# Optimization experiments

Hardware: AMD Instinct MI355X
Metric: run time of the kernel (lower is better)

The kernel has to match this reference:

```python
import jax, jax.numpy as jnp
import numpy as np

HEAD_NUM = 16
ROPE_BASE = 10000.0


def _rotate_half(x):
    # interleaved pairs: (x0,x1,x2,x3,...) -> (-x1,x0,-x3,x2,...)
    x_even = x[..., ::2]
    x_odd = x[..., 1::2]
    return jnp.stack((-x_odd, x_even), axis=-1).reshape(x.shape)


def _rope_cos_sin(seq_len, head_dim):
    half = head_dim // 2
    inv_freq = 1.0 / (ROPE_BASE ** (jnp.arange(half, dtype=jnp.float32) / half))
    t = jnp.arange(seq_len, dtype=jnp.float32)
    freqs = t[:, None] * inv_freq[None, :]            # [S, half]
    cos = jnp.repeat(jnp.cos(freqs), 2, axis=-1)       # [S, D]
    sin = jnp.repeat(jnp.sin(freqs), 2, axis=-1)       # [S, D]
    return cos, sin


def setup_inputs() -> dict:
    key = jax.random.key(0)
    ks = jax.random.split(key, 9)
    B, S, H = 2, 2048, 2048
    std = 1.0 / np.sqrt(H)
    return {
        "x": jax.random.normal(ks[0], (B, S, H), jnp.float32),
        "Wq": jax.random.normal(ks[1], (H, H), jnp.float32) * std,
        "bq": jax.random.normal(ks[2], (H,), jnp.float32) * std,
        "Wk": jax.random.normal(ks[3], (H, H), jnp.float32) * std,
        "bk": jax.random.normal(ks[4], (H,), jnp.float32) * std,
        "Wv": jax.random.normal(ks[5], (H, H), jnp.float32) * std,
        "bv": jax.random.normal(ks[6], (H,), jnp.float32) * std,
        "Wo": jax.random.normal(ks[7], (H, H), jnp.float32) * std,
        "bo": jax.random.normal(ks[8], (H,), jnp.float32) * std,
    }


def reference(x, Wq, bq, Wk, bk, Wv, bv, Wo, bo):
    B, S, H = x.shape
    nh = HEAD_NUM
    d = H // nh
    scale = jnp.float32(np.sqrt(d))

    def proj(W, b):
        y = x @ W.T + b                                 # torch Linear: x W^T + b
        return y.reshape(B, S, nh, d).transpose(0, 2, 1, 3)  # [B, nh, S, d]

    Q = proj(Wq, bq)
    K = proj(Wk, bk)
    V = proj(Wv, bv)

    cos, sin = _rope_cos_sin(S, d)                      # [S, d]
    Q = Q * cos + _rotate_half(Q) * sin
    K = K * cos + _rotate_half(K) * sin

    scores = jnp.einsum("bhqd,bhkd->bhqk", Q, K) / scale  # [B, nh, S, S]
    causal = jnp.tril(jnp.ones((S, S), dtype=bool))
    scores = jnp.where(causal, scores, jnp.float32(-jnp.inf))
    attn = jax.nn.softmax(scores, axis=-1)
    out = jnp.einsum("bhqk,bhkd->bhqd", attn, V)        # [B, nh, S, d]
    out = out.transpose(0, 2, 1, 3).reshape(B, S, H)
    return out @ Wo.T + bo
```

## Files before the change

### kernel.cpp

```cpp
#include <hip/hip_runtime.h>
#include <math.h>

typedef __bf16 bf16x8 __attribute__((ext_vector_type(8)));
typedef float floatx4 __attribute__((ext_vector_type(4)));

__device__ __forceinline__ unsigned short f32_to_bf16(float f) {
  unsigned int u = __float_as_uint(f);
  u = u + 0x7FFFu + ((u >> 16) & 1u);
  return (unsigned short)(u >> 16);
}
__device__ __forceinline__ float bf16_to_f32(unsigned short s) {
  return __uint_as_float(((unsigned int)s) << 16);
}

__device__ __forceinline__ void gld_lds16(const unsigned short* g,
                                          unsigned short* l) {
  __builtin_amdgcn_global_load_lds(
      (const __attribute__((address_space(1))) unsigned int*)g,
      (__attribute__((address_space(3))) unsigned int*)l, 16, 0, 0);
}

__global__ void cast_kernel(const float* __restrict__ in,
                            unsigned short* __restrict__ out, int n4) {
  int i = blockIdx.x * blockDim.x + threadIdx.x;
  if (i >= n4) return;
  const float4 v = reinterpret_cast<const float4*>(in)[i];
  ushort4 o;
  o.x = f32_to_bf16(v.x); o.y = f32_to_bf16(v.y);
  o.z = f32_to_bf16(v.z); o.w = f32_to_bf16(v.w);
  reinterpret_cast<ushort4*>(out)[i] = o;
}

__global__ void rope_table_kernel(float2* __restrict__ tab, int total) {
  int idx = blockIdx.x * blockDim.x + threadIdx.x;
  if (idx >= total) return;
  const int s = idx >> 6, i = idx & 63;
  const float inv = powf(10000.0f, -(float)i * (1.0f / 64.0f));
  const float ang = (float)s * inv;
  tab[idx] = make_float2(cosf(ang), sinf(ang));
}

template <int EPI>
__global__ __launch_bounds__(256) void gemm_fused(
    const unsigned short* __restrict__ A, const unsigned short* __restrict__ B,
    const float* __restrict__ bias, float* __restrict__ Cf,
    unsigned short* __restrict__ Cb, const float2* __restrict__ tab,
    float scl, int M, int N, int K, int S) {
  __shared__ unsigned short As[128 * 64];
  __shared__ unsigned short Bs[128 * 64];
  const int t = threadIdx.x;
  const int lane = t & 63;
  const int w = t >> 6;
  const int bm = blockIdx.y * 128;
  const int bn = blockIdx.x * 128;
  const int wm = (w & 1) * 64;
  const int wn = (w >> 1) * 64;
  const int m16 = lane & 15;
  const int quad = lane >> 4;
  const int key = m16 & 7;

  const int lr = lane >> 3;
  const int lc = ((lane & 7) ^ lr) * 8;

  floatx4 acc[4][4];
#pragma unroll
  for (int i = 0; i < 4; ++i)
#pragma unroll
    for (int j = 0; j < 4; ++j) acc[i][j] = floatx4{0.f, 0.f, 0.f, 0.f};

  const unsigned short* Abase = A + (size_t)(bm + w * 32 + lr) * K + lc;
  const unsigned short* Bbase = B + (size_t)(bn + w * 32 + lr) * K + lc;

  for (int k0 = 0; k0 < K; k0 += 64) {
    __syncthreads();
#pragma unroll
    for (int it = 0; it < 4; ++it) {
      gld_lds16(Abase + (size_t)it * 8 * K + k0, &As[(w * 4 + it) * 512]);
      gld_lds16(Bbase + (size_t)it * 8 * K + k0, &Bs[(w * 4 + it) * 512]);
    }
    __syncthreads();
#pragma unroll
    for (int ks = 0; ks < 64; ks += 32) {
      const int ck = ks >> 3;
      bf16x8 af[4], bfr[4];
#pragma unroll
      for (int i = 0; i < 4; ++i)
        af[i] = *reinterpret_cast<const bf16x8*>(
            &As[(wm + i * 16 + m16) * 64 + ((ck | quad) ^ key) * 8]);
#pragma unroll
      for (int j = 0; j < 4; ++j)
        bfr[j] = *reinterpret_cast<const bf16x8*>(
            &Bs[(wn + j * 16 + m16) * 64 + ((ck | quad) ^ key) * 8]);
#pragma unroll
      for (int i = 0; i < 4; ++i)
#pragma unroll
        for (int j = 0; j < 4; ++j)
          acc[i][j] = __builtin_amdgcn_mfma_f32_16x16x32_bf16(
              af[i], bfr[j], acc[i][j], 0, 0, 0);
    }
  }

#pragma unroll
  for (int i = 0; i < 4; ++i) {
    const int rbase = bm + wm + i * 16 + quad * 4;
#pragma unroll
    for (int j = 0; j < 4; ++j) {
      const int col = bn + wn + j * 16 + m16;
      const float bv = bias[col];
      if (EPI == 0) {
#pragma unroll
        for (int r = 0; r < 4; ++r)
          Cf[(size_t)(rbase + r) * N + col] = acc[i][j][r] + bv;
      } else if (EPI == 1) {
        const int pi = (col & 127) >> 1;
#pragma unroll
        for (int r = 0; r < 4; ++r) {
          const int row = rbase + r;
          const int s = row & (S - 1);
          const float v = acc[i][j][r] + bv;
          const float vp = __shfl_xor(v, 1);
          const float2 cs = tab[s * 64 + pi];
          const float oe = (v * cs.x - vp * cs.y) * scl;
          const float oo = (vp * cs.x + v * cs.y) * scl;
          if ((m16 & 1) == 0) {
            const unsigned pk =
                (unsigned)f32_to_bf16(oe) | ((unsigned)f32_to_bf16(oo) << 16);
            *reinterpret_cast<unsigned*>(Cb + (size_t)row * N + col) = pk;
          }
        }
      } else {
        const int b = rbase >> 11;
        const int s = rbase & (S - 1);
        ushort4 pk;
        pk.x = f32_to_bf16(acc[i][j][0] + bv);
        pk.y = f32_to_bf16(acc[i][j][1] + bv);
        pk.z = f32_to_bf16(acc[i][j][2] + bv);
        pk.w = f32_to_bf16(acc[i][j][3] + bv);
        *reinterpret_cast<ushort4*>(
            Cb + ((size_t)((b << 11) + col)) * S + s) = pk;
      }
    }
  }
}

constexpr int F_BQ = 128, F_BK = 64, F_DH = 128;
constexpr int KS_STR = 136;
constexpr int VS_STR = 72;
constexpr int PS_STR = 72;

__global__ __launch_bounds__(256, 2) void fattn_kernel(
    const unsigned short* __restrict__ Qb, const unsigned short* __restrict__ Kb,
    const unsigned short* __restrict__ Vtb, unsigned short* __restrict__ Ob,
    int S, int H, int nh) {
  __shared__ unsigned short Ks[F_BK * KS_STR];
  __shared__ unsigned short Vts[F_DH * VS_STR];
  __shared__ unsigned short Ps[F_BQ * PS_STR];

  const int t = threadIdx.x;
  const int lane = t & 63;
  const int w = t >> 6;
  const int l15 = lane & 15;
  const int quad = lane >> 4;

  const int i = blockIdx.x;
  const int bh = i & 31;
  const int qt = (i < 256) ? (i >> 5) : (15 - ((i - 256) >> 5));
  const int h = bh & 15;
  const int b = bh >> 4;
  const int q0 = qt * F_BQ;

  const unsigned short* Qrow = Qb + ((size_t)(b * S + q0)) * H + h * F_DH;
  const unsigned short* Krow = Kb + ((size_t)b * S) * H + h * F_DH;
  const unsigned short* Vtrow = Vtb + ((size_t)bh * F_DH) * S;
  unsigned short* Orow = Ob + ((size_t)(b * S + q0)) * H + h * F_DH;

  bf16x8 aq[2][4];
#pragma unroll
  for (int qg = 0; qg < 2; ++qg)
#pragma unroll
    for (int ks = 0; ks < 4; ++ks)
      aq[qg][ks] = *reinterpret_cast<const bf16x8*>(
          Qrow + (size_t)(w * 32 + qg * 16 + l15) * H + ks * 32 + quad * 8);

  floatx4 oacc[2][8];
#pragma unroll
  for (int qg = 0; qg < 2; ++qg)
#pragma unroll
    for (int dj = 0; dj < 8; ++dj) oacc[qg][dj] = floatx4{0.f, 0.f, 0.f, 0.f};
  float lpart[2][4] = {{0.f, 0.f, 0.f, 0.f}, {0.f, 0.f, 0.f, 0.f}};
  int qrow[2][4];
#pragma unroll
  for (int qg = 0; qg < 2; ++qg)
#pragma unroll
    for (int r = 0; r < 4; ++r)
      qrow[qg][r] = q0 + w * 32 + qg * 16 + quad * 4 + r;

  const int ntile = q0 / F_BK + 2;
  for (int tile = 0; tile < ntile; ++tile) {
    const int k0 = tile * F_BK;
    __syncthreads();
    {
      const int kt = t >> 2, c0 = (t & 3) * 32;
      const unsigned short* g = Krow + (size_t)(k0 + kt) * H + c0;
#pragma unroll
      for (int ii = 0; ii < 4; ++ii)
        *reinterpret_cast<uint4*>(&Ks[kt * KS_STR + c0 + ii * 8]) =
            *reinterpret_cast<const uint4*>(g + ii * 8);
    }
    {
      const int d = t >> 1, c0 = (t & 1) * 32;
      const unsigned short* g = Vtrow + (size_t)d * S + k0 + c0;
#pragma unroll
      for (int ii = 0; ii < 4; ++ii)
        *reinterpret_cast<uint4*>(&Vts[d * VS_STR + c0 + ii * 8]) =
            *reinterpret_cast<const uint4*>(g + ii * 8);
    }
    __syncthreads();

    floatx4 sacc[2][4];
#pragma unroll
    for (int qg = 0; qg < 2; ++qg)
#pragma unroll
      for (int j = 0; j < 4; ++j) sacc[qg][j] = floatx4{0.f, 0.f, 0.f, 0.f};
#pragma unroll
    for (int j = 0; j < 4; ++j) {
      bf16x8 bk[4];
#pragma unroll
      for (int ks = 0; ks < 4; ++ks)
        bk[ks] = *reinterpret_cast<const bf16x8*>(
            &Ks[(j * 16 + l15) * KS_STR + ks * 32 + quad * 8]);
#pragma unroll
      for (int qg = 0; qg < 2; ++qg)
#pragma unroll
        for (int ks = 0; ks < 4; ++ks)
          sacc[qg][j] = __builtin_amdgcn_mfma_f32_16x16x32_bf16(
              aq[qg][ks], bk[ks], sacc[qg][j], 0, 0, 0);
    }

#pragma unroll
    for (int qg = 0; qg < 2; ++qg)
#pragma unroll
      for (int j = 0; j < 4; ++j) {
        const int ktg = k0 + j * 16 + l15;
#pragma unroll
        for (int r = 0; r < 4; ++r) {
          const float p =
              (ktg <= qrow[qg][r]) ? exp2f(sacc[qg][j][r]) : 0.0f;
          lpart[qg][r] += p;
          Ps[(w * 32 + qg * 16 + quad * 4 + r) * PS_STR + j * 16 + l15] =
              f32_to_bf16(p);
        }
      }

#pragma unroll
    for (int ks2 = 0; ks2 < 2; ++ks2) {
      bf16x8 ap[2];
#pragma unroll
      for (int qg = 0; qg < 2; ++qg)
        ap[qg] = *reinterpret_cast<const bf16x8*>(
            &Ps[(w * 32 + qg * 16 + l15) * PS_STR + ks2 * 32 + quad * 8]);
#pragma unroll
      for (int dj = 0; dj < 8; ++dj) {
        const bf16x8 bv = *reinterpret_cast<const bf16x8*>(
            &Vts[(dj * 16 + l15) * VS_STR + ks2 * 32 + quad * 8]);
#pragma unroll
        for (int qg = 0; qg < 2; ++qg)
          oacc[qg][dj] = __builtin_amdgcn_mfma_f32_16x16x32_bf16(
              ap[qg], bv, oacc[qg][dj], 0, 0, 0);
      }
    }
  }

#pragma unroll
  for (int qg = 0; qg < 2; ++qg)
#pragma unroll
    for (int r = 0; r < 4; ++r) {
      float l = lpart[qg][r];
      l += __shfl_xor(l, 1);
      l += __shfl_xor(l, 2);
      l += __shfl_xor(l, 4);
      l += __shfl_xor(l, 8);
      const float linv = 1.0f / l;
      unsigned short* orow =
          Orow + (size_t)(w * 32 + qg * 16 + quad * 4 + r) * H;
#pragma unroll
      for (int dj = 0; dj < 8; ++dj)
        orow[dj * 16 + l15] = f32_to_bf16(oacc[qg][dj][r] * linv);
    }
}

extern "C" void kernel_launch(void* const* d_in, const int* in_sizes, int n_in,
                              void* d_out, int out_size, void* d_ws,
                              size_t ws_size, hipStream_t stream) {
  const float* x  = (const float*)d_in[0];
  const float* Wq = (const float*)d_in[1];
  const float* bq = (const float*)d_in[2];
  const float* Wk = (const float*)d_in[3];
  const float* bk = (const float*)d_in[4];
  const float* Wv = (const float*)d_in[5];
  const float* bv = (const float*)d_in[6];
  const float* Wo = (const float*)d_in[7];
  const float* bo = (const float*)d_in[8];
  float* out = (float*)d_out;

  const int B = 2, S = 2048, H = 2048, nh = 16;
  const int M = B * S;

  unsigned short* Wqb = (unsigned short*)d_ws;
  unsigned short* Wkb = Wqb + (size_t)H * H;
  unsigned short* Wvb = Wkb + (size_t)H * H;
  unsigned short* Wob = Wvb + (size_t)H * H;
  unsigned short* xb  = Wob + (size_t)H * H;
  unsigned short* Qbb = xb + (size_t)M * H;
  unsigned short* Kbb = Qbb + (size_t)M * H;
  unsigned short* Vtb = Kbb + (size_t)M * H;
  unsigned short* Ob  = Vtb + (size_t)M * H;
  float2* tab = (float2*)(Ob + (size_t)M * H);

  const int cast_w4 = H * H / 4;
  const int cast_x4 = M * H / 4;
  const int tab_n = S * 64;

  rope_table_kernel<<<dim3(tab_n / 256), dim3(256), 0, stream>>>(tab, tab_n);
  cast_kernel<<<dim3(cast_x4 / 256), dim3(256), 0, stream>>>(x, xb, cast_x4);
  cast_kernel<<<dim3(cast_w4 / 256), dim3(256), 0, stream>>>(Wq, Wqb, cast_w4);
  cast_kernel<<<dim3(cast_w4 / 256), dim3(256), 0, stream>>>(Wk, Wkb, cast_w4);
  cast_kernel<<<dim3(cast_w4 / 256), dim3(256), 0, stream>>>(Wv, Wvb, cast_w4);
  cast_kernel<<<dim3(cast_w4 / 256), dim3(256), 0, stream>>>(Wo, Wob, cast_w4);

  dim3 ggrid(H / 128, M / 128);
  const float qscale = 0.08838834764831845f * 1.4426950408889634f;

  gemm_fused<1><<<ggrid, dim3(256), 0, stream>>>(
      xb, Wqb, bq, nullptr, Qbb, tab, qscale, M, H, H, S);
  gemm_fused<1><<<ggrid, dim3(256), 0, stream>>>(
      xb, Wkb, bk, nullptr, Kbb, tab, 1.0f, M, H, H, S);
  gemm_fused<2><<<ggrid, dim3(256), 0, stream>>>(
      xb, Wvb, bv, nullptr, Vtb, nullptr, 1.0f, M, H, H, S);

  fattn_kernel<<<dim3((S / F_BQ) * B * nh), dim3(256), 0, stream>>>(
      Qbb, Kbb, Vtb, Ob, S, H, nh);

  gemm_fused<0><<<ggrid, dim3(256), 0, stream>>>(
      Ob, Wob, bo, out, nullptr, nullptr, 1.0f, M, H, H, S);
}
```

Baseline: 446.2 us.

## Batch QKV GEMMs and weight casts, prefetch K/V tiles into registers

```diff
diff --git a/kernel.cpp b/kernel.cpp
--- a/kernel.cpp
+++ b/kernel.cpp
@@ -24,6 +24,31 @@
                             unsigned short* __restrict__ out, int n4) {
   int i = blockIdx.x * blockDim.x + threadIdx.x;
   if (i >= n4) return;
+  const float4 v = reinterpret_cast<const float4*>(in)[i];
+  ushort4 o;
+  o.x = f32_to_bf16(v.x); o.y = f32_to_bf16(v.y);
+  o.z = f32_to_bf16(v.z); o.w = f32_to_bf16(v.w);
+  reinterpret_cast<ushort4*>(out)[i] = o;
+}
+
+__global__ void cast4_kernel(const float* __restrict__ a,
+                             const float* __restrict__ b,
+                             const float* __restrict__ c,
+                             const float* __restrict__ d,
+                             unsigned short* __restrict__ oa,
+                             unsigned short* __restrict__ ob,
+                             unsigned short* __restrict__ oc,
+                             unsigned short* __restrict__ od, int n4) {
+  int i = blockIdx.x * blockDim.x + threadIdx.x;
+  if (i >= n4) return;
+  const float* in;
+  unsigned short* out;
+  switch (blockIdx.y) {
+    case 0: in = a; out = oa; break;
+    case 1: in = b; out = ob; break;
+    case 2: in = c; out = oc; break;
+    default: in = d; out = od; break;
+  }
   const float4 v = reinterpret_cast<const float4*>(in)[i];
   ushort4 o;
   o.x = f32_to_bf16(v.x); o.y = f32_to_bf16(v.y);
@@ -106,18 +131,97 @@
 #pragma unroll
     for (int j = 0; j < 4; ++j) {
       const int col = bn + wn + j * 16 + m16;
-      const float bv = bias[col];
+      const float bvv = bias[col];
       if (EPI == 0) {
 #pragma unroll
         for (int r = 0; r < 4; ++r)
-          Cf[(size_t)(rbase + r) * N + col] = acc[i][j][r] + bv;
-      } else if (EPI == 1) {
+          Cf[(size_t)(rbase + r) * N + col] = acc[i][j][r] + bvv;
+      }
+    }
+  }
+}
+
+__global__ __launch_bounds__(256) void gemm_qkv(
+    const unsigned short* __restrict__ A, const unsigned short* __restrict__ Bq,
+    const unsigned short* __restrict__ Bk, const unsigned short* __restrict__ Bv,
+    const float* __restrict__ biasq, const float* __restrict__ biask,
+    const float* __restrict__ biasv, unsigned short* __restrict__ Qb,
+    unsigned short* __restrict__ Kb, unsigned short* __restrict__ Vtb,
+    const float2* __restrict__ tab, float qscale, int M, int N, int K, int S) {
+  __shared__ unsigned short As[128 * 64];
+  __shared__ unsigned short Bs[128 * 64];
+  const int t = threadIdx.x;
+  const int lane = t & 63;
+  const int w = t >> 6;
+  const int z = blockIdx.z;
+  const int bm = blockIdx.y * 128;
+  const int bn = blockIdx.x * 128;
+  const int wm = (w & 1) * 64;
+  const int wn = (w >> 1) * 64;
+  const int m16 = lane & 15;
+  const int quad = lane >> 4;
+  const int key = m16 & 7;
+
+  const int lr = lane >> 3;
+  const int lc = ((lane & 7) ^ lr) * 8;
+
+  const unsigned short* B = (z == 0) ? Bq : ((z == 1) ? Bk : Bv);
+  const float* bias = (z == 0) ? biasq : ((z == 1) ? biask : biasv);
+  unsigned short* Cb = (z == 0) ? Qb : ((z == 1) ? Kb : Vtb);
+  const float scl = (z == 0) ? qscale : 1.0f;
+
+  floatx4 acc[4][4];
+#pragma unroll
+  for (int i = 0; i < 4; ++i)
+#pragma unroll
+    for (int j = 0; j < 4; ++j) acc[i][j] = floatx4{0.f, 0.f, 0.f, 0.f};
+
+  const unsigned short* Abase = A + (size_t)(bm + w * 32 + lr) * K + lc;
+  const unsigned short* Bbase = B + (size_t)(bn + w * 32 + lr) * K + lc;
+
+  for (int k0 = 0; k0 < K; k0 += 64) {
+    __syncthreads();
+#pragma unroll
+    for (int it = 0; it < 4; ++it) {
+      gld_lds16(Abase + (size_t)it * 8 * K + k0, &As[(w * 4 + it) * 512]);
+      gld_lds16(Bbase + (size_t)it * 8 * K + k0, &Bs[(w * 4 + it) * 512]);
+    }
+    __syncthreads();
+#pragma unroll
+    for (int ks = 0; ks < 64; ks += 32) {
+      const int ck = ks >> 3;
+      bf16x8 af[4], bfr[4];
+#pragma unroll
+      for (int i = 0; i < 4; ++i)
+        af[i] = *reinterpret_cast<const bf16x8*>(
+            &As[(wm + i * 16 + m16) * 64 + ((ck | quad) ^ key) * 8]);
+#pragma unroll
+      for (int j = 0; j < 4; ++j)
+        bfr[j] = *reinterpret_cast<const bf16x8*>(
+            &Bs[(wn + j * 16 + m16) * 64 + ((ck | quad) ^ key) * 8]);
+#pragma unroll
+      for (int i = 0; i < 4; ++i)
+#pragma unroll
+        for (int j = 0; j < 4; ++j)
+          acc[i][j] = __builtin_amdgcn_mfma_f32_16x16x32_bf16(
+              af[i], bfr[j], acc[i][j], 0, 0, 0);
+    }
+  }
+
+#pragma unroll
+  for (int i = 0; i < 4; ++i) {
+    const int rbase = bm + wm + i * 16 + quad * 4;
+#pragma unroll
+    for (int j = 0; j < 4; ++j) {
+      const int col = bn + wn + j * 16 + m16;
+      const float bvv = bias[col];
+      if (z != 2) {
         const int pi = (col & 127) >> 1;
 #pragma unroll
         for (int r = 0; r < 4; ++r) {
           const int row = rbase + r;
           const int s = row & (S - 1);
-          const float v = acc[i][j][r] + bv;
+          const float v = acc[i][j][r] + bvv;
           const float vp = __shfl_xor(v, 1);
           const float2 cs = tab[s * 64 + pi];
           const float oe = (v * cs.x - vp * cs.y) * scl;
@@ -132,10 +236,10 @@
         const int b = rbase >> 11;
         const int s = rbase & (S - 1);
         ushort4 pk;
-        pk.x = f32_to_bf16(acc[i][j][0] + bv);
-        pk.y = f32_to_bf16(acc[i][j][1] + bv);
-        pk.z = f32_to_bf16(acc[i][j][2] + bv);
-        pk.w = f32_to_bf16(acc[i][j][3] + bv);
+        pk.x = f32_to_bf16(acc[i][j][0] + bvv);
+        pk.y = f32_to_bf16(acc[i][j][1] + bvv);
+        pk.z = f32_to_bf16(acc[i][j][2] + bvv);
+        pk.w = f32_to_bf16(acc[i][j][3] + bvv);
         *reinterpret_cast<ushort4*>(
             Cb + ((size_t)((b << 11) + col)) * S + s) = pk;
       }
@@ -174,6 +278,11 @@
   const unsigned short* Vtrow = Vtb + ((size_t)bh * F_DH) * S;
   unsigned short* Orow = Ob + ((size_t)(b * S + q0)) * H + h * F_DH;
 
+  const int kt = t >> 2, ck0 = (t & 3) * 32;
+  const int vd = t >> 1, cv0 = (t & 1) * 32;
+  const unsigned short* Kg = Krow + (size_t)kt * H + ck0;
+  const unsigned short* Vg = Vtrow + (size_t)vd * S + cv0;
+
   bf16x8 aq[2][4];
 #pragma unroll
   for (int qg = 0; qg < 2; ++qg)
@@ -182,6 +291,14 @@
       aq[qg][ks] = *reinterpret_cast<const bf16x8*>(
           Qrow + (size_t)(w * 32 + qg * 16 + l15) * H + ks * 32 + quad * 8);
 
+  uint4 kreg[4], vreg[4];
+#pragma unroll
+  for (int ii = 0; ii < 4; ++ii)
+    kreg[ii] = *reinterpret_cast<const uint4*>(Kg + ii * 8);
+#pragma unroll
+  for (int ii = 0; ii < 4; ++ii)
+    vreg[ii] = *reinterpret_cast<const uint4*>(Vg + ii * 8);
+
   floatx4 oacc[2][8];
 #pragma unroll
   for (int qg = 0; qg < 2; ++qg)
@@ -199,23 +316,23 @@
   for (int tile = 0; tile < ntile; ++tile) {
     const int k0 = tile * F_BK;
     __syncthreads();
-    {
-      const int kt = t >> 2, c0 = (t & 3) * 32;
-      const unsigned short* g = Krow + (size_t)(k0 + kt) * H + c0;
+#pragma unroll
+    for (int ii = 0; ii < 4; ++ii)
+      *reinterpret_cast<uint4*>(&Ks[kt * KS_STR + ck0 + ii * 8]) = kreg[ii];
+#pragma unroll
+    for (int ii = 0; ii < 4; ++ii)
+      *reinterpret_cast<uint4*>(&Vts[vd * VS_STR + cv0 + ii * 8]) = vreg[ii];
+    __syncthreads();
+
+    if (tile + 1 < ntile) {
+      const int k1 = (tile + 1) * F_BK;
 #pragma unroll
       for (int ii = 0; ii < 4; ++ii)
-        *reinterpret_cast<uint4*>(&Ks[kt * KS_STR + c0 + ii * 8]) =
-            *reinterpret_cast<const uint4*>(g + ii * 8);
-    }
-    {
-      const int d = t >> 1, c0 = (t & 1) * 32;
-      const unsigned short* g = Vtrow + (size_t)d * S + k0 + c0;
+        kreg[ii] = *reinterpret_cast<const uint4*>(Kg + (size_t)k1 * H + ii * 8);
 #pragma unroll
       for (int ii = 0; ii < 4; ++ii)
-        *reinterpret_cast<uint4*>(&Vts[d * VS_STR + c0 + ii * 8]) =
-            *reinterpret_cast<const uint4*>(g + ii * 8);
-    }
-    __syncthreads();
+        vreg[ii] = *reinterpret_cast<const uint4*>(Vg + k1 + ii * 8);
+    }
 
     floatx4 sacc[2][4];
 #pragma unroll
@@ -323,24 +440,17 @@
 
   rope_table_kernel<<<dim3(tab_n / 256), dim3(256), 0, stream>>>(tab, tab_n);
   cast_kernel<<<dim3(cast_x4 / 256), dim3(256), 0, stream>>>(x, xb, cast_x4);
-  cast_kernel<<<dim3(cast_w4 / 256), dim3(256), 0, stream>>>(Wq, Wqb, cast_w4);
-  cast_kernel<<<dim3(cast_w4 / 256), dim3(256), 0, stream>>>(Wk, Wkb, cast_w4);
-  cast_kernel<<<dim3(cast_w4 / 256), dim3(256), 0, stream>>>(Wv, Wvb, cast_w4);
-  cast_kernel<<<dim3(cast_w4 / 256), dim3(256), 0, stream>>>(Wo, Wob, cast_w4);
-
-  dim3 ggrid(H / 128, M / 128);
+  cast4_kernel<<<dim3(cast_w4 / 256, 4), dim3(256), 0, stream>>>(
+      Wq, Wk, Wv, Wo, Wqb, Wkb, Wvb, Wob, cast_w4);
+
   const float qscale = 0.08838834764831845f * 1.4426950408889634f;
 
-  gemm_fused<1><<<ggrid, dim3(256), 0, stream>>>(
-      xb, Wqb, bq, nullptr, Qbb, tab, qscale, M, H, H, S);
-  gemm_fused<1><<<ggrid, dim3(256), 0, stream>>>(
-      xb, Wkb, bk, nullptr, Kbb, tab, 1.0f, M, H, H, S);
-  gemm_fused<2><<<ggrid, dim3(256), 0, stream>>>(
-      xb, Wvb, bv, nullptr, Vtb, nullptr, 1.0f, M, H, H, S);
+  gemm_qkv<<<dim3(H / 128, M / 128, 3), dim3(256), 0, stream>>>(
+      xb, Wqb, Wkb, Wvb, bq, bk, bv, Qbb, Kbb, Vtb, tab, qscale, M, H, H, S);
 
   fattn_kernel<<<dim3((S / F_BQ) * B * nh), dim3(256), 0, stream>>>(
       Qbb, Kbb, Vtb, Ob, S, H, nh);
 
-  gemm_fused<0><<<ggrid, dim3(256), 0, stream>>>(
+  gemm_fused<0><<<dim3(H / 128, M / 128), dim3(256), 0, stream>>>(
       Ob, Wob, bo, out, nullptr, nullptr, 1.0f, M, H, H, S);
 }
```

After: 473.3 us. 6.1% more time.
